# Kernel optimization log

Hardware: AMD Instinct MI355X
Metric: run time of the kernel (lower is better)

Reference implementation:

```python
import jax, jax.numpy as jnp
import numpy as np

B, T, IN, H, OUT = 256, 100, 128, 1024, 35
BITS = 4
SLOPE = 25.0
THR_H = 1.0
THR_O = 1.0
BETA1, BETA2, BETA3, BETA4 = 0.9, 0.85, 0.8, 0.95


def fake_quant(w, w_min, w_max, bits=BITS):
    # FakeQuantize in training mode: STE -> forward value is quantized, grad passes through clamp
    levels = 2 ** bits
    scale = (w_max - w_min) / (levels - 1)
    wc = jnp.clip(w, w_min, w_max)
    q = jnp.round((wc - w_min) / scale) * scale + w_min
    return wc + jax.lax.stop_gradient(q - wc)


@jax.custom_vjp
def spike(x):
    # Heaviside forward, fast-sigmoid surrogate backward (snn.surrogate.fast_sigmoid)
    return (x > 0).astype(x.dtype)

def _spike_fwd(x):
    return (x > 0).astype(x.dtype), x

def _spike_bwd(x, g):
    return (g / (SLOPE * jnp.abs(x) + 1.0) ** 2,)

spike.defvjp(_spike_fwd, _spike_bwd)


def lif_step(cur, mem, beta, thr, reset_mechanism):
    # snntorch Leaky (reset_delay semantics): reset computed from previous mem, detached
    reset = jax.lax.stop_gradient((mem > thr).astype(cur.dtype))
    base = beta * mem + cur
    if reset_mechanism == "subtract":
        mem_new = base - reset * thr
    else:  # "zero"
        mem_new = base - reset * base
    spk = spike(mem_new - thr)
    return spk, mem_new


def setup_inputs() -> dict:
    key = jax.random.key(0)
    ks = jax.random.split(key, 5)
    x = jax.random.normal(ks[0], (B, T, IN), dtype=jnp.float32)
    # QuantLinear init: uniform(w_min, w_max); fc1 uses (-0.5, 0.5), others (0.001, 1.0)
    w1 = jax.random.uniform(ks[1], (H, IN), minval=-0.5, maxval=0.5, dtype=jnp.float32)
    w2 = jax.random.uniform(ks[2], (H, H), minval=0.001, maxval=1.0, dtype=jnp.float32)
    w3 = jax.random.uniform(ks[3], (H, H), minval=0.001, maxval=1.0, dtype=jnp.float32)
    w4 = jax.random.uniform(ks[4], (OUT, H), minval=0.001, maxval=1.0, dtype=jnp.float32)
    return {"x": x, "w1": w1, "w2": w2, "w3": w3, "w4": w4}


def reference(x, w1, w2, w3, w4):
    # hoist weight quantization out of the time loop (identical math each step)
    q1 = fake_quant(w1, -0.5, 0.5)
    q2 = fake_quant(w2, 0.001, 1.0)
    q3 = fake_quant(w3, 0.001, 1.0)
    q4 = fake_quant(w4, 0.001, 1.0)
    xs = jnp.transpose(x, (1, 0, 2)) / 15.0  # [T, B, IN]
    Bx = x.shape[0]

    def step(carry, xt):
        m1, m2, m3, m4 = carry
        s1, m1 = lif_step(xt @ q1.T, m1, BETA1, THR_H, "subtract")
        s2, m2 = lif_step(s1 @ q2.T, m2, BETA2, THR_H, "subtract")
        s3, m3 = lif_step(s2 @ q3.T, m3, BETA3, THR_H, "subtract")
        s4, m4 = lif_step(s3 @ q4.T, m4, BETA4, THR_O, "zero")
        return (m1, m2, m3, m4), (s1, s2, s3, s4, m4)

    init = (jnp.zeros((Bx, H), x.dtype), jnp.zeros((Bx, H), x.dtype),
            jnp.zeros((Bx, H), x.dtype), jnp.zeros((Bx, OUT), x.dtype))
    _, (spk1, spk2, spk3, spk4, mem4) = jax.lax.scan(step, init, xs)
    # stacked along time dim 0, matching torch.stack(dim=0)
    return spk1, spk2, spk3, spk4, mem4
```

## Files before the change

kernel.cpp:

```cpp
#include <hip/hip_runtime.h>
#include <stdint.h>

#define NB  256
#define NT  100
#define NIN 128
#define NH  1024
#define NOUT 35

#define O_SPK2 26214400ull
#define O_SPK3 52428800ull
#define O_SPK4 78643200ull
#define O_MEM4 79539200ull

#define WS_XT   0ull
#define WS_Q1T  13107200ull
#define WS_K2T  13631488ull
#define WS_K3T  14680064ull
#define WS_K4T  15728640ull
#define WS_RS2  15777792ull
#define WS_RS3  15781888ull
#define WS_RS4  15785984ull

#define S2C ((float)((1.0 - 0.001) / 15.0))
#define S1C ((float)(1.0 / 15.0))

__global__ void k_prep(const float* __restrict__ x, const float* __restrict__ w1,
                       const float* __restrict__ w2, const float* __restrict__ w3,
                       const float* __restrict__ w4, uint8_t* __restrict__ ws)
{
  long long id = (long long)blockIdx.x * 256 + threadIdx.x;
  if (id < 1048576) {
    int i = (int)(id >> 10), j = (int)(id & 1023);
    float wv = w2[(size_t)j * 1024 + i];
    float wc = fminf(fmaxf(wv, 0.001f), 1.0f);
    ws[WS_K2T + id] = (uint8_t)(int)rintf((wc - 0.001f) / S2C);
    return;
  }
  id -= 1048576;
  if (id < 1048576) {
    int i = (int)(id >> 10), j = (int)(id & 1023);
    float wv = w3[(size_t)j * 1024 + i];
    float wc = fminf(fmaxf(wv, 0.001f), 1.0f);
    ws[WS_K3T + id] = (uint8_t)(int)rintf((wc - 0.001f) / S2C);
    return;
  }
  id -= 1048576;
  if (id < 49152) {
    int i = (int)(id / 48), j = (int)(id % 48);
    uint8_t v = 0;
    if (j < NOUT) {
      float wv = w4[(size_t)j * 1024 + i];
      float wc = fminf(fmaxf(wv, 0.001f), 1.0f);
      v = (uint8_t)(int)rintf((wc - 0.001f) / S2C);
    }
    ws[WS_K4T + id] = v;
    return;
  }
  id -= 49152;
  if (id < 131072) {
    int i = (int)(id >> 10), j = (int)(id & 1023);
    float wv = w1[(size_t)j * 128 + i];
    float wc = fminf(fmaxf(wv, -0.5f), 0.5f);
    float q = rintf((wc + 0.5f) / S1C) * S1C - 0.5f;
    ((float*)(ws + WS_Q1T))[id] = q;
    return;
  }
  id -= 131072;
  if (id < 3276800) {
    int row = (int)(id >> 7), i = (int)(id & 127);
    int tt = row >> 8, bb = row & 255;
    ((float*)(ws + WS_XT))[id] = x[((size_t)bb * NT + tt) * NIN + i] / 15.0f;
  }
}

__global__ void k_rowsum(const float* __restrict__ w2, const float* __restrict__ w3,
                         const float* __restrict__ w4, uint8_t* __restrict__ ws)
{
  int bid = blockIdx.x, tid = threadIdx.x;
  const float* W;
  uint32_t* o;
  if (bid < 1024)      { W = w2 + (size_t)bid * 1024;          o = (uint32_t*)(ws + WS_RS2) + bid; }
  else if (bid < 2048) { W = w3 + (size_t)(bid - 1024) * 1024; o = (uint32_t*)(ws + WS_RS3) + (bid - 1024); }
  else                 { W = w4 + (size_t)(bid - 2048) * 1024; o = (uint32_t*)(ws + WS_RS4) + (bid - 2048); }
  uint32_t s = 0;
  for (int i = tid; i < 1024; i += 256) {
    float wc = fminf(fmaxf(W[i], 0.001f), 1.0f);
    s += (uint32_t)(int)rintf((wc - 0.001f) / S2C);
  }
  #pragma unroll
  for (int off = 32; off; off >>= 1) s += (uint32_t)__shfl_down((int)s, off);
  __shared__ uint32_t red[4];
  if ((tid & 63) == 0) red[tid >> 6] = s;
  __syncthreads();
  if (tid == 0) *o = red[0] + red[1] + red[2] + red[3];
}

__global__ __launch_bounds__(512, 1) void k_spk1(const float* __restrict__ xt,
                                                 const float* __restrict__ q1T,
                                                 float* __restrict__ out)
{
  __shared__ float xs[25 * 128];
  const int b = blockIdx.x;
  const int tid = threadIdx.x;
  float m1a = 0.f, m1b = 0.f;

  for (int c = 0; c < 4; ++c) {
    __syncthreads();
    {
      int e = tid;
      int tt = e >> 5, iq = e & 31;
      ((float4*)xs)[e] = *(const float4*)(xt + ((size_t)(c * 25 + tt) * NB + b) * NIN + iq * 4);
      e = tid + 512;
      if (e < 800) {
        tt = e >> 5; iq = e & 31;
        ((float4*)xs)[e] = *(const float4*)(xt + ((size_t)(c * 25 + tt) * NB + b) * NIN + iq * 4);
      }
    }
    __syncthreads();

    float acc0[25], acc1[25];
    #pragma unroll
    for (int tt = 0; tt < 25; ++tt) { acc0[tt] = 0.f; acc1[tt] = 0.f; }

    for (int ib = 0; ib < 16; ++ib) {
      float q0[8], q1v[8];
      #pragma unroll
      for (int u = 0; u < 8; ++u) {
        q0[u]  = q1T[(size_t)(ib * 8 + u) * NH + tid];
        q1v[u] = q1T[(size_t)(ib * 8 + u) * NH + tid + 512];
      }
      #pragma unroll
      for (int tt = 0; tt < 25; ++tt) {
        const float4 xa = *(const float4*)&xs[tt * 128 + ib * 8];
        const float4 xb = *(const float4*)&xs[tt * 128 + ib * 8 + 4];
        acc0[tt] = fmaf(xa.x, q0[0], acc0[tt]);
        acc0[tt] = fmaf(xa.y, q0[1], acc0[tt]);
        acc0[tt] = fmaf(xa.z, q0[2], acc0[tt]);
        acc0[tt] = fmaf(xa.w, q0[3], acc0[tt]);
        acc0[tt] = fmaf(xb.x, q0[4], acc0[tt]);
        acc0[tt] = fmaf(xb.y, q0[5], acc0[tt]);
        acc0[tt] = fmaf(xb.z, q0[6], acc0[tt]);
        acc0[tt] = fmaf(xb.w, q0[7], acc0[tt]);
        acc1[tt] = fmaf(xa.x, q1v[0], acc1[tt]);
        acc1[tt] = fmaf(xa.y, q1v[1], acc1[tt]);
        acc1[tt] = fmaf(xa.z, q1v[2], acc1[tt]);
        acc1[tt] = fmaf(xa.w, q1v[3], acc1[tt]);
        acc1[tt] = fmaf(xb.x, q1v[4], acc1[tt]);
        acc1[tt] = fmaf(xb.y, q1v[5], acc1[tt]);
        acc1[tt] = fmaf(xb.z, q1v[6], acc1[tt]);
        acc1[tt] = fmaf(xb.w, q1v[7], acc1[tt]);
      }
    }
    #pragma unroll
    for (int tt = 0; tt < 25; ++tt) {
      const int t = c * 25 + tt;
      const size_t row = ((size_t)t * NB + b) * (size_t)NH;
      float rst0 = m1a > 1.0f ? 1.0f : 0.0f;
      m1a = fmaf(0.9f, m1a, acc0[tt]) - rst0;
      out[row + tid] = ((m1a - 1.0f) > 0.0f) ? 1.0f : 0.0f;
      float rst1 = m1b > 1.0f ? 1.0f : 0.0f;
      m1b = fmaf(0.9f, m1b, acc1[tt]) - rst1;
      out[row + tid + 512] = ((m1b - 1.0f) > 0.0f) ? 1.0f : 0.0f;
    }
  }
}

__global__ __launch_bounds__(1024, 1) void k_main(
    const uint8_t* __restrict__ k2T, const uint8_t* __restrict__ k3T,
    const uint8_t* __restrict__ k4T, const uint32_t* __restrict__ rs2,
    const uint32_t* __restrict__ rs3, const uint32_t* __restrict__ rs4,
    float* __restrict__ out)
{
  const int b = blockIdx.x;
  const int tid = threadIdx.x;
  const int lane = tid & 63;
  const int wave = tid >> 6;

  __shared__ uint16_t list[1024];
  __shared__ uint4    pEa4[1024];
  __shared__ uint4    pOa4[1024];
  __shared__ uint4    wcnt4[4];
  __shared__ uint32_t lpos;
  uint32_t* pEa  = (uint32_t*)pEa4;
  uint32_t* pOa  = (uint32_t*)pOa4;
  uint32_t* wcnt = (uint32_t*)wcnt4;

  float m2 = 0.f, m3 = 0.f, m4 = 0.f;
  const uint32_t r2v = rs2[tid];
  const uint32_t r3v = rs3[tid];
  const uint32_t r4v = (tid < NOUT) ? rs4[tid] : 0u;

  auto sumcnt = [&]() -> uint32_t {
    uint4 a0 = wcnt4[0], a1 = wcnt4[1], a2 = wcnt4[2], a3 = wcnt4[3];
    return a0.x + a0.y + a0.z + a0.w + a1.x + a1.y + a1.z + a1.w +
           a2.x + a2.y + a2.z + a2.w + a3.x + a3.y + a3.z + a3.w;
  };

  auto writeList = [&](uint64_t cw) {
    uint32_t cnt = (uint32_t)__popcll(cw);
    uint32_t bs = 0;
    if (lane == 0) bs = atomicAdd(&lpos, cnt);
    bs = (uint32_t)__shfl((int)bs, 0);
    if ((cw >> lane) & 1ull)
      list[bs + (uint32_t)__popcll(cw & ((1ull << lane) - 1ull))] = (uint16_t)tid;
  };

  auto gatherBig = [&](const uint8_t* __restrict__ mat, uint32_t nLv) {
    uint32_t aE0=0,aE1=0,aE2=0,aE3=0,aO0=0,aO1=0,aO2=0,aO3=0;
    const uint8_t* bp = mat + (lane << 4);
    uint32_t a = (uint32_t)wave;
    for (; a + 16 < nLv; a += 32) {
      uint32_t i0 = (uint32_t)__builtin_amdgcn_readfirstlane((int)list[a]);
      uint32_t i1 = (uint32_t)__builtin_amdgcn_readfirstlane((int)list[a + 16]);
      const uint4 w0 = *(const uint4*)(bp + ((size_t)i0 << 10));
      const uint4 w1 = *(const uint4*)(bp + ((size_t)i1 << 10));
      aE0 += w0.x & 0x00FF00FFu; aO0 += (w0.x >> 8) & 0x00FF00FFu;
      aE1 += w0.y & 0x00FF00FFu; aO1 += (w0.y >> 8) & 0x00FF00FFu;
      aE2 += w0.z & 0x00FF00FFu; aO2 += (w0.z >> 8) & 0x00FF00FFu;
      aE3 += w0.w & 0x00FF00FFu; aO3 += (w0.w >> 8) & 0x00FF00FFu;
      aE0 += w1.x & 0x00FF00FFu; aO0 += (w1.x >> 8) & 0x00FF00FFu;
      aE1 += w1.y & 0x00FF00FFu; aO1 += (w1.y >> 8) & 0x00FF00FFu;
      aE2 += w1.z & 0x00FF00FFu; aO2 += (w1.z >> 8) & 0x00FF00FFu;
      aE3 += w1.w & 0x00FF00FFu; aO3 += (w1.w >> 8) & 0x00FF00FFu;
    }
    if (a < nLv) {
      uint32_t i0 = (uint32_t)__builtin_amdgcn_readfirstlane((int)list[a]);
      const uint4 w0 = *(const uint4*)(bp + ((size_t)i0 << 10));
      aE0 += w0.x & 0x00FF00FFu; aO0 += (w0.x >> 8) & 0x00FF00FFu;
      aE1 += w0.y & 0x00FF00FFu; aO1 += (w0.y >> 8) & 0x00FF00FFu;
      aE2 += w0.z & 0x00FF00FFu; aO2 += (w0.z >> 8) & 0x00FF00FFu;
      aE3 += w0.w & 0x00FF00FFu; aO3 += (w0.w >> 8) & 0x00FF00FFu;
    }
    const int basei = (wave << 8) + (lane << 2);
    *(uint4*)&pEa[basei] = make_uint4(aE0, aE1, aE2, aE3);
    *(uint4*)&pOa[basei] = make_uint4(aO0, aO1, aO2, aO3);
  };

  auto gsum = [&](int jn) -> uint32_t {
    int w = jn >> 2, sh = (jn & 2) << 3;
    const uint32_t* P = (jn & 1) ? pOa : pEa;
    uint32_t s = 0;
    #pragma unroll
    for (int g = 0; g < 16; ++g) s += (P[(g << 8) + w] >> sh) & 0xffffu;
    return s;
  };

  float s1v = out[(size_t)b * NH + tid];
  uint32_t nT, nL; bool cm;

  for (int t = 0; t < NT; ++t) {
    const size_t rowH = ((size_t)t * NB + b) * (size_t)NH;
    const size_t rowO = ((size_t)t * NB + b) * (size_t)NOUT;

    bool sA = s1v > 0.5f;
    {
      int tn = (t + 1 < NT) ? (t + 1) : t;
      s1v = out[((size_t)tn * NB + b) * (size_t)NH + tid];
    }
    uint64_t b1 = __ballot(sA);
    if (tid == 0) lpos = 0;
    if (lane == 0) wcnt[wave] = (uint32_t)__popcll(b1);
    __syncthreads();
    nT = sumcnt(); cm = nT > 512; nL = cm ? 1024u - nT : nT;
    writeList(cm ? ~b1 : b1);
    __syncthreads();
    const uint32_t n1 = nT, nl1 = nL; const bool cm1 = cm;
    if (nl1) gatherBig(k2T, nl1);
    __syncthreads();

    bool sp;
    {
      uint32_t gsv = nl1 ? gsum(tid) : 0u;
      uint32_t K = cm1 ? (r2v - gsv) : gsv;
      float cur = fmaf(S2C, (float)K, 0.001f * (float)n1);
      float rst = m2 > 1.0f ? 1.0f : 0.0f;
      m2 = fmaf(0.85f, m2, cur) - rst;
      sp = (m2 - 1.0f) > 0.0f;
      out[O_SPK2 + rowH + tid] = sp ? 1.0f : 0.0f;
    }
    uint64_t b2 = __ballot(sp);
    if (tid == 0) lpos = 0;
    if (lane == 0) wcnt[wave] = (uint32_t)__popcll(b2);
    __syncthreads();
    nT = sumcnt(); cm = nT > 512; nL = cm ? 1024u - nT : nT;
    writeList(cm ? ~b2 : b2);
    __syncthreads();
    const uint32_t n2 = nT, nl2 = nL; const bool cm2 = cm;
    if (nl2) gatherBig(k3T, nl2);
    __syncthreads();

    {
      uint32_t gsv = nl2 ? gsum(tid) : 0u;
      uint32_t K = cm2 ? (r3v - gsv) : gsv;
      float cur = fmaf(S2C, (float)K, 0.001f * (float)n2);
      float rst = m3 > 1.0f ? 1.0f : 0.0f;
      m3 = fmaf(0.8f, m3, cur) - rst;
      sp = (m3 - 1.0f) > 0.0f;
      out[O_SPK3 + rowH + tid] = sp ? 1.0f : 0.0f;
    }
    uint64_t b3 = __ballot(sp);
    if (tid == 0) lpos = 0;
    if (lane == 0) wcnt[wave] = (uint32_t)__popcll(b3);
    __syncthreads();
    nT = sumcnt(); cm = nT > 512; nL = cm ? 1024u - nT : nT;
    writeList(cm ? ~b3 : b3);
    __syncthreads();
    const uint32_t n3 = nT, nl3 = nL; const bool cm3 = cm;

    if (nl3 && lane < 3) {
      uint32_t aE0=0,aE1=0,aE2=0,aE3=0,aO0=0,aO1=0,aO2=0,aO3=0;
      const uint8_t* bp = k4T + (lane << 4);
      for (uint32_t a = (uint32_t)wave; a < nl3; a += 16) {
        uint32_t i0 = (uint32_t)__builtin_amdgcn_readfirstlane((int)list[a]);
        const uint4 w0 = *(const uint4*)(bp + (size_t)i0 * 48u);
        aE0 += w0.x & 0x00FF00FFu; aO0 += (w0.x >> 8) & 0x00FF00FFu;
        aE1 += w0.y & 0x00FF00FFu; aO1 += (w0.y >> 8) & 0x00FF00FFu;
        aE2 += w0.z & 0x00FF00FFu; aO2 += (w0.z >> 8) & 0x00FF00FFu;
        aE3 += w0.w & 0x00FF00FFu; aO3 += (w0.w >> 8) & 0x00FF00FFu;
      }
      const int basei = (wave << 8) + (lane << 2);
      *(uint4*)&pEa[basei] = make_uint4(aE0, aE1, aE2, aE3);
      *(uint4*)&pOa[basei] = make_uint4(aO0, aO1, aO2, aO3);
    }
    __syncthreads();

    if (tid < NOUT) {
      uint32_t gsv = nl3 ? gsum(tid) : 0u;
      uint32_t K = cm3 ? (r4v - gsv) : gsv;
      float cur = fmaf(S2C, (float)K, 0.001f * (float)n3);
      float rst = m4 > 1.0f ? 1.0f : 0.0f;
      float bsv = fmaf(0.95f, m4, cur);
      m4 = (rst > 0.0f) ? 0.0f : bsv;
      out[O_SPK4 + rowO + tid] = ((m4 - 1.0f) > 0.0f) ? 1.0f : 0.0f;
      out[O_MEM4 + rowO + tid] = m4;
    }
  }
}

extern "C" void kernel_launch(void* const* d_in, const int* in_sizes, int n_in,
                              void* d_out, int out_size, void* d_ws, size_t ws_size,
                              hipStream_t stream)
{
  const float* x  = (const float*)d_in[0];
  const float* w1 = (const float*)d_in[1];
  const float* w2 = (const float*)d_in[2];
  const float* w3 = (const float*)d_in[3];
  const float* w4 = (const float*)d_in[4];
  float* out = (float*)d_out;
  uint8_t* ws = (uint8_t*)d_ws;
  hipLaunchKernelGGL(k_prep,   dim3(21696), dim3(256), 0, stream, x, w1, w2, w3, w4, ws);
  hipLaunchKernelGGL(k_rowsum, dim3(2083),  dim3(256), 0, stream, w2, w3, w4, ws);
  hipLaunchKernelGGL(k_spk1,   dim3(256),   dim3(512), 0, stream,
                     (const float*)(ws + WS_XT), (const float*)(ws + WS_Q1T), out);
  hipLaunchKernelGGL(k_main,   dim3(256),   dim3(1024), 0, stream,
                     ws + WS_K2T, ws + WS_K3T, ws + WS_K4T,
                     (const uint32_t*)(ws + WS_RS2), (const uint32_t*)(ws + WS_RS3),
                     (const uint32_t*)(ws + WS_RS4), out);
}
```

Before: 701.1 us.

## Halve main kernel block size, compute row sums in-kernel, replace atomic list build

The recurrent kernel now runs 512 threads per block, each owning two hidden neurons, so every gather step covers four list entries per wave with a stride of 8. The separate row-sum kernel is removed, and each block recomputes the quantized column sums at startup by gathering all rows of the weight tables. The shared-memory atomic list append is replaced by a deterministic prefix sum over the per-wave counts. This cuts one launch and the atomics and improves memory-level parallelism. In exchange it doubles per-thread work, halves the number of waves available to hide latency, and adds a redundant full-matrix sweep per block.

```diff
diff --git a/kernel.cpp b/kernel.cpp
--- a/kernel.cpp
+++ b/kernel.cpp
@@ -17,9 +17,6 @@
 #define WS_K2T  13631488ull
 #define WS_K3T  14680064ull
 #define WS_K4T  15728640ull
-#define WS_RS2  15777792ull
-#define WS_RS3  15781888ull
-#define WS_RS4  15785984ull
 
 #define S2C ((float)((1.0 - 0.001) / 15.0))
 #define S1C ((float)(1.0 / 15.0))
@@ -71,28 +68,6 @@
     int tt = row >> 8, bb = row & 255;
     ((float*)(ws + WS_XT))[id] = x[((size_t)bb * NT + tt) * NIN + i] / 15.0f;
   }
-}
-
-__global__ void k_rowsum(const float* __restrict__ w2, const float* __restrict__ w3,
-                         const float* __restrict__ w4, uint8_t* __restrict__ ws)
-{
-  int bid = blockIdx.x, tid = threadIdx.x;
-  const float* W;
-  uint32_t* o;
-  if (bid < 1024)      { W = w2 + (size_t)bid * 1024;          o = (uint32_t*)(ws + WS_RS2) + bid; }
-  else if (bid < 2048) { W = w3 + (size_t)(bid - 1024) * 1024; o = (uint32_t*)(ws + WS_RS3) + (bid - 1024); }
-  else                 { W = w4 + (size_t)(bid - 2048) * 1024; o = (uint32_t*)(ws + WS_RS4) + (bid - 2048); }
-  uint32_t s = 0;
-  for (int i = tid; i < 1024; i += 256) {
-    float wc = fminf(fmaxf(W[i], 0.001f), 1.0f);
-    s += (uint32_t)(int)rintf((wc - 0.001f) / S2C);
-  }
-  #pragma unroll
-  for (int off = 32; off; off >>= 1) s += (uint32_t)__shfl_down((int)s, off);
-  __shared__ uint32_t red[4];
-  if ((tid & 63) == 0) red[tid >> 6] = s;
-  __syncthreads();
-  if (tid == 0) *o = red[0] + red[1] + red[2] + red[3];
 }
 
 __global__ __launch_bounds__(512, 1) void k_spk1(const float* __restrict__ xt,
@@ -165,11 +140,15 @@
   }
 }
 
-__global__ __launch_bounds__(1024, 1) void k_main(
+#define ACC(V) do { \
+  aE0 += (V).x & 0x00FF00FFu; aO0 += ((V).x >> 8) & 0x00FF00FFu; \
+  aE1 += (V).y & 0x00FF00FFu; aO1 += ((V).y >> 8) & 0x00FF00FFu; \
+  aE2 += (V).z & 0x00FF00FFu; aO2 += ((V).z >> 8) & 0x00FF00FFu; \
+  aE3 += (V).w & 0x00FF00FFu; aO3 += ((V).w >> 8) & 0x00FF00FFu; } while (0)
+
+__global__ __launch_bounds__(512, 1) void k_main(
     const uint8_t* __restrict__ k2T, const uint8_t* __restrict__ k3T,
-    const uint8_t* __restrict__ k4T, const uint32_t* __restrict__ rs2,
-    const uint32_t* __restrict__ rs3, const uint32_t* __restrict__ rs4,
-    float* __restrict__ out)
+    const uint8_t* __restrict__ k4T, float* __restrict__ out)
 {
   const int b = blockIdx.x;
   const int tid = threadIdx.x;
@@ -177,151 +156,207 @@
   const int wave = tid >> 6;
 
   __shared__ uint16_t list[1024];
-  __shared__ uint4    pEa4[1024];
-  __shared__ uint4    pOa4[1024];
-  __shared__ uint4    wcnt4[4];
-  __shared__ uint32_t lpos;
+  __shared__ uint4    pEa4[512];
+  __shared__ uint4    pOa4[512];
+  __shared__ uint4    wcnt4[2];
   uint32_t* pEa  = (uint32_t*)pEa4;
   uint32_t* pOa  = (uint32_t*)pOa4;
   uint32_t* wcnt = (uint32_t*)wcnt4;
 
-  float m2 = 0.f, m3 = 0.f, m4 = 0.f;
-  const uint32_t r2v = rs2[tid];
-  const uint32_t r3v = rs3[tid];
-  const uint32_t r4v = (tid < NOUT) ? rs4[tid] : 0u;
-
-  auto sumcnt = [&]() -> uint32_t {
-    uint4 a0 = wcnt4[0], a1 = wcnt4[1], a2 = wcnt4[2], a3 = wcnt4[3];
-    return a0.x + a0.y + a0.z + a0.w + a1.x + a1.y + a1.z + a1.w +
-           a2.x + a2.y + a2.z + a2.w + a3.x + a3.y + a3.z + a3.w;
-  };
-
-  auto writeList = [&](uint64_t cw) {
-    uint32_t cnt = (uint32_t)__popcll(cw);
-    uint32_t bs = 0;
-    if (lane == 0) bs = atomicAdd(&lpos, cnt);
-    bs = (uint32_t)__shfl((int)bs, 0);
-    if ((cw >> lane) & 1ull)
-      list[bs + (uint32_t)__popcll(cw & ((1ull << lane) - 1ull))] = (uint16_t)tid;
+  float m2[2] = {0.f, 0.f}, m3[2] = {0.f, 0.f}, m4 = 0.f;
+  uint32_t nT, nL; bool cm;
+
+  auto buildList = [&](uint64_t bA, uint64_t bB) {
+    const uint4 c0 = wcnt4[0], c1 = wcnt4[1];
+    nT = c0.x + c0.y + c0.z + c0.w + c1.x + c1.y + c1.z + c1.w;
+    cm = nT > 512;
+    nL = cm ? (1024u - nT) : nT;
+    uint32_t pre = 0;
+    pre += (wave > 0) ? c0.x : 0u;  pre += (wave > 1) ? c0.y : 0u;
+    pre += (wave > 2) ? c0.z : 0u;  pre += (wave > 3) ? c0.w : 0u;
+    pre += (wave > 4) ? c1.x : 0u;  pre += (wave > 5) ? c1.y : 0u;
+    pre += (wave > 6) ? c1.z : 0u;
+    const uint32_t bs = cm ? ((uint32_t)(wave << 7) - pre) : pre;
+    const uint64_t cA = cm ? ~bA : bA;
+    const uint64_t cB = cm ? ~bB : bB;
+    const uint64_t ltm = (1ull << lane) - 1ull;
+    if ((cA >> lane) & 1ull)
+      list[bs + (uint32_t)__popcll(cA & ltm)] = (uint16_t)tid;
+    if ((cB >> lane) & 1ull)
+      list[bs + (uint32_t)__popcll(cA) + (uint32_t)__popcll(cB & ltm)] = (uint16_t)(tid + 512);
   };
 
   auto gatherBig = [&](const uint8_t* __restrict__ mat, uint32_t nLv) {
     uint32_t aE0=0,aE1=0,aE2=0,aE3=0,aO0=0,aO1=0,aO2=0,aO3=0;
     const uint8_t* bp = mat + (lane << 4);
     uint32_t a = (uint32_t)wave;
-    for (; a + 16 < nLv; a += 32) {
+    for (; a + 24 < nLv; a += 32) {
       uint32_t i0 = (uint32_t)__builtin_amdgcn_readfirstlane((int)list[a]);
-      uint32_t i1 = (uint32_t)__builtin_amdgcn_readfirstlane((int)list[a + 16]);
-      const uint4 w0 = *(const uint4*)(bp + ((size_t)i0 << 10));
-      const uint4 w1 = *(const uint4*)(bp + ((size_t)i1 << 10));
-      aE0 += w0.x & 0x00FF00FFu; aO0 += (w0.x >> 8) & 0x00FF00FFu;
-      aE1 += w0.y & 0x00FF00FFu; aO1 += (w0.y >> 8) & 0x00FF00FFu;
-      aE2 += w0.z & 0x00FF00FFu; aO2 += (w0.z >> 8) & 0x00FF00FFu;
-      aE3 += w0.w & 0x00FF00FFu; aO3 += (w0.w >> 8) & 0x00FF00FFu;
-      aE0 += w1.x & 0x00FF00FFu; aO0 += (w1.x >> 8) & 0x00FF00FFu;
-      aE1 += w1.y & 0x00FF00FFu; aO1 += (w1.y >> 8) & 0x00FF00FFu;
-      aE2 += w1.z & 0x00FF00FFu; aO2 += (w1.z >> 8) & 0x00FF00FFu;
-      aE3 += w1.w & 0x00FF00FFu; aO3 += (w1.w >> 8) & 0x00FF00FFu;
-    }
-    if (a < nLv) {
+      uint32_t i1 = (uint32_t)__builtin_amdgcn_readfirstlane((int)list[a + 8]);
+      uint32_t i2 = (uint32_t)__builtin_amdgcn_readfirstlane((int)list[a + 16]);
+      uint32_t i3 = (uint32_t)__builtin_amdgcn_readfirstlane((int)list[a + 24]);
+      const uint4 v0 = *(const uint4*)(bp + ((size_t)i0 << 10));
+      const uint4 v1 = *(const uint4*)(bp + ((size_t)i1 << 10));
+      const uint4 v2 = *(const uint4*)(bp + ((size_t)i2 << 10));
+      const uint4 v3 = *(const uint4*)(bp + ((size_t)i3 << 10));
+      ACC(v0); ACC(v1); ACC(v2); ACC(v3);
+    }
+    for (; a < nLv; a += 8) {
       uint32_t i0 = (uint32_t)__builtin_amdgcn_readfirstlane((int)list[a]);
-      const uint4 w0 = *(const uint4*)(bp + ((size_t)i0 << 10));
-      aE0 += w0.x & 0x00FF00FFu; aO0 += (w0.x >> 8) & 0x00FF00FFu;
-      aE1 += w0.y & 0x00FF00FFu; aO1 += (w0.y >> 8) & 0x00FF00FFu;
-      aE2 += w0.z & 0x00FF00FFu; aO2 += (w0.z >> 8) & 0x00FF00FFu;
-      aE3 += w0.w & 0x00FF00FFu; aO3 += (w0.w >> 8) & 0x00FF00FFu;
+      const uint4 v0 = *(const uint4*)(bp + ((size_t)i0 << 10));
+      ACC(v0);
     }
     const int basei = (wave << 8) + (lane << 2);
     *(uint4*)&pEa[basei] = make_uint4(aE0, aE1, aE2, aE3);
     *(uint4*)&pOa[basei] = make_uint4(aO0, aO1, aO2, aO3);
   };
 
+  auto gatherAll = [&](const uint8_t* __restrict__ mat) {
+    uint32_t aE0=0,aE1=0,aE2=0,aE3=0,aO0=0,aO1=0,aO2=0,aO3=0;
+    const uint8_t* bp = mat + (lane << 4);
+    for (uint32_t a = (uint32_t)wave; a + 24 < 1024u; a += 32) {
+      const uint4 v0 = *(const uint4*)(bp + ((size_t)a << 10));
+      const uint4 v1 = *(const uint4*)(bp + ((size_t)(a + 8) << 10));
+      const uint4 v2 = *(const uint4*)(bp + ((size_t)(a + 16) << 10));
+      const uint4 v3 = *(const uint4*)(bp + ((size_t)(a + 24) << 10));
+      ACC(v0); ACC(v1); ACC(v2); ACC(v3);
+    }
+    const int basei = (wave << 8) + (lane << 2);
+    *(uint4*)&pEa[basei] = make_uint4(aE0, aE1, aE2, aE3);
+    *(uint4*)&pOa[basei] = make_uint4(aO0, aO1, aO2, aO3);
+  };
+
+  auto gather4 = [&](uint32_t nLv) {
+    uint32_t aE0=0,aE1=0,aE2=0,aE3=0,aO0=0,aO1=0,aO2=0,aO3=0;
+    const uint8_t* bp = k4T + (lane << 4);
+    uint32_t a = (uint32_t)wave;
+    for (; a + 24 < nLv; a += 32) {
+      uint32_t i0 = (uint32_t)__builtin_amdgcn_readfirstlane((int)list[a]);
+      uint32_t i1 = (uint32_t)__builtin_amdgcn_readfirstlane((int)list[a + 8]);
+      uint32_t i2 = (uint32_t)__builtin_amdgcn_readfirstlane((int)list[a + 16]);
+      uint32_t i3 = (uint32_t)__builtin_amdgcn_readfirstlane((int)list[a + 24]);
+      const uint4 v0 = *(const uint4*)(bp + (size_t)i0 * 48u);
+      const uint4 v1 = *(const uint4*)(bp + (size_t)i1 * 48u);
+      const uint4 v2 = *(const uint4*)(bp + (size_t)i2 * 48u);
+      const uint4 v3 = *(const uint4*)(bp + (size_t)i3 * 48u);
+      ACC(v0); ACC(v1); ACC(v2); ACC(v3);
+    }
+    for (; a < nLv; a += 8) {
+      uint32_t i0 = (uint32_t)__builtin_amdgcn_readfirstlane((int)list[a]);
+      const uint4 v0 = *(const uint4*)(bp + (size_t)i0 * 48u);
+      ACC(v0);
+    }
+    const int basei = (wave << 8) + (lane << 2);
+    *(uint4*)&pEa[basei] = make_uint4(aE0, aE1, aE2, aE3);
+    *(uint4*)&pOa[basei] = make_uint4(aO0, aO1, aO2, aO3);
+  };
+
+  auto gather4All = [&]() {
+    uint32_t aE0=0,aE1=0,aE2=0,aE3=0,aO0=0,aO1=0,aO2=0,aO3=0;
+    const uint8_t* bp = k4T + (lane << 4);
+    for (uint32_t a = (uint32_t)wave; a + 24 < 1024u; a += 32) {
+      const uint4 v0 = *(const uint4*)(bp + (size_t)a * 48u);
+      const uint4 v1 = *(const uint4*)(bp + (size_t)(a + 8) * 48u);
+      const uint4 v2 = *(const uint4*)(bp + (size_t)(a + 16) * 48u);
+      const uint4 v3 = *(const uint4*)(bp + (size_t)(a + 24) * 48u);
+      ACC(v0); ACC(v1); ACC(v2); ACC(v3);
+    }
+    const int basei = (wave << 8) + (lane << 2);
+    *(uint4*)&pEa[basei] = make_uint4(aE0, aE1, aE2, aE3);
+    *(uint4*)&pOa[basei] = make_uint4(aO0, aO1, aO2, aO3);
+  };
+
   auto gsum = [&](int jn) -> uint32_t {
-    int w = jn >> 2, sh = (jn & 2) << 3;
+    const int w = jn >> 2, sh = (jn & 2) << 3;
     const uint32_t* P = (jn & 1) ? pOa : pEa;
     uint32_t s = 0;
     #pragma unroll
-    for (int g = 0; g < 16; ++g) s += (P[(g << 8) + w] >> sh) & 0xffffu;
-    return s;
-  };
-
-  float s1v = out[(size_t)b * NH + tid];
-  uint32_t nT, nL; bool cm;
+    for (int g = 0; g < 8; ++g) s += P[(g << 8) + w];
+    return (s >> sh) & 0xffffu;
+  };
+
+  gatherAll(k2T);
+  __syncthreads();
+  uint32_t r2[2]; r2[0] = gsum(tid); r2[1] = gsum(tid + 512);
+  __syncthreads();
+  gatherAll(k3T);
+  __syncthreads();
+  uint32_t r3[2]; r3[0] = gsum(tid); r3[1] = gsum(tid + 512);
+  __syncthreads();
+  if (lane < 3) gather4All();
+  __syncthreads();
+  const uint32_t r4v = (tid < NOUT) ? gsum(tid) : 0u;
+
+  float s1a = out[(size_t)b * NH + tid];
+  float s1b = out[(size_t)b * NH + tid + 512];
 
   for (int t = 0; t < NT; ++t) {
     const size_t rowH = ((size_t)t * NB + b) * (size_t)NH;
     const size_t rowO = ((size_t)t * NB + b) * (size_t)NOUT;
 
-    bool sA = s1v > 0.5f;
+    bool sA = s1a > 0.5f, sB = s1b > 0.5f;
     {
       int tn = (t + 1 < NT) ? (t + 1) : t;
-      s1v = out[((size_t)tn * NB + b) * (size_t)NH + tid];
-    }
-    uint64_t b1 = __ballot(sA);
-    if (tid == 0) lpos = 0;
-    if (lane == 0) wcnt[wave] = (uint32_t)__popcll(b1);
-    __syncthreads();
-    nT = sumcnt(); cm = nT > 512; nL = cm ? 1024u - nT : nT;
-    writeList(cm ? ~b1 : b1);
+      size_t rowN = ((size_t)tn * NB + b) * (size_t)NH;
+      s1a = out[rowN + tid];
+      s1b = out[rowN + tid + 512];
+    }
+    uint64_t bA = __ballot(sA), bB = __ballot(sB);
+    if (lane == 0) wcnt[wave] = (uint32_t)(__popcll(bA) + __popcll(bB));
+    __syncthreads();
+    buildList(bA, bB);
     __syncthreads();
     const uint32_t n1 = nT, nl1 = nL; const bool cm1 = cm;
     if (nl1) gatherBig(k2T, nl1);
     __syncthreads();
 
-    bool sp;
     {
-      uint32_t gsv = nl1 ? gsum(tid) : 0u;
-      uint32_t K = cm1 ? (r2v - gsv) : gsv;
-      float cur = fmaf(S2C, (float)K, 0.001f * (float)n1);
-      float rst = m2 > 1.0f ? 1.0f : 0.0f;
-      m2 = fmaf(0.85f, m2, cur) - rst;
-      sp = (m2 - 1.0f) > 0.0f;
-      out[O_SPK2 + rowH + tid] = sp ? 1.0f : 0.0f;
-    }
-    uint64_t b2 = __ballot(sp);
-    if (tid == 0) lpos = 0;
-    if (lane == 0) wcnt[wave] = (uint32_t)__popcll(b2);
-    __syncthreads();
-    nT = sumcnt(); cm = nT > 512; nL = cm ? 1024u - nT : nT;
-    writeList(cm ? ~b2 : b2);
+      float nb = 0.001f * (float)n1;
+      #pragma unroll
+      for (int c = 0; c < 2; ++c) {
+        int j = (c << 9) + tid;
+        uint32_t gsv = nl1 ? gsum(j) : 0u;
+        uint32_t K = cm1 ? (r2[c] - gsv) : gsv;
+        float cur = fmaf(S2C, (float)K, nb);
+        float rst = m2[c] > 1.0f ? 1.0f : 0.0f;
+        m2[c] = fmaf(0.85f, m2[c], cur) - rst;
+        bool sp = (m2[c] - 1.0f) > 0.0f;
+        out[O_SPK2 + rowH + j] = sp ? 1.0f : 0.0f;
+        if (c == 0) sA = sp; else sB = sp;
+      }
+    }
+    bA = __ballot(sA); bB = __ballot(sB);
+    if (lane == 0) wcnt[wave] = (uint32_t)(__popcll(bA) + __popcll(bB));
+    __syncthreads();
+    buildList(bA, bB);
     __syncthreads();
     const uint32_t n2 = nT, nl2 = nL; const bool cm2 = cm;
     if (nl2) gatherBig(k3T, nl2);
     __syncthreads();
 
     {
-      uint32_t gsv = nl2 ? gsum(tid) : 0u;
-      uint32_t K = cm2 ? (r3v - gsv) : gsv;
-      float cur = fmaf(S2C, (float)K, 0.001f * (float)n2);
-      float rst = m3 > 1.0f ? 1.0f : 0.0f;
-      m3 = fmaf(0.8f, m3, cur) - rst;
-      sp = (m3 - 1.0f) > 0.0f;
-      out[O_SPK3 + rowH + tid] = sp ? 1.0f : 0.0f;
-    }
-    uint64_t b3 = __ballot(sp);
-    if (tid == 0) lpos = 0;
-    if (lane == 0) wcnt[wave] = (uint32_t)__popcll(b3);
-    __syncthreads();
-    nT = sumcnt(); cm = nT > 512; nL = cm ? 1024u - nT : nT;
-    writeList(cm ? ~b3 : b3);
+      float nb = 0.001f * (float)n2;
+      #pragma unroll
+      for (int c = 0; c < 2; ++c) {
+        int j = (c << 9) + tid;
+        uint32_t gsv = nl2 ? gsum(j) : 0u;
+        uint32_t K = cm2 ? (r3[c] - gsv) : gsv;
+        float cur = fmaf(S2C, (float)K, nb);
+        float rst = m3[c] > 1.0f ? 1.0f : 0.0f;
+        m3[c] = fmaf(0.8f, m3[c], cur) - rst;
+        bool sp = (m3[c] - 1.0f) > 0.0f;
+        out[O_SPK3 + rowH + j] = sp ? 1.0f : 0.0f;
+        if (c == 0) sA = sp; else sB = sp;
+      }
+    }
+    bA = __ballot(sA); bB = __ballot(sB);
+    if (lane == 0) wcnt[wave] = (uint32_t)(__popcll(bA) + __popcll(bB));
+    __syncthreads();
+    buildList(bA, bB);
     __syncthreads();
     const uint32_t n3 = nT, nl3 = nL; const bool cm3 = cm;
 
-    if (nl3 && lane < 3) {
-      uint32_t aE0=0,aE1=0,aE2=0,aE3=0,aO0=0,aO1=0,aO2=0,aO3=0;
-      const uint8_t* bp = k4T + (lane << 4);
-      for (uint32_t a = (uint32_t)wave; a < nl3; a += 16) {
-        uint32_t i0 = (uint32_t)__builtin_amdgcn_readfirstlane((int)list[a]);
-        const uint4 w0 = *(const uint4*)(bp + (size_t)i0 * 48u);
-        aE0 += w0.x & 0x00FF00FFu; aO0 += (w0.x >> 8) & 0x00FF00FFu;
-        aE1 += w0.y & 0x00FF00FFu; aO1 += (w0.y >> 8) & 0x00FF00FFu;
-        aE2 += w0.z & 0x00FF00FFu; aO2 += (w0.z >> 8) & 0x00FF00FFu;
-        aE3 += w0.w & 0x00FF00FFu; aO3 += (w0.w >> 8) & 0x00FF00FFu;
-      }
-      const int basei = (wave << 8) + (lane << 2);
-      *(uint4*)&pEa[basei] = make_uint4(aE0, aE1, aE2, aE3);
-      *(uint4*)&pOa[basei] = make_uint4(aO0, aO1, aO2, aO3);
-    }
+    if (nl3 && lane < 3) gather4(nl3);
     __syncthreads();
 
     if (tid < NOUT) {
@@ -336,6 +371,7 @@
     }
   }
 }
+#undef ACC
 
 extern "C" void kernel_launch(void* const* d_in, const int* in_sizes, int n_in,
                               void* d_out, int out_size, void* d_ws, size_t ws_size,
@@ -348,12 +384,9 @@
   const float* w4 = (const float*)d_in[4];
   float* out = (float*)d_out;
   uint8_t* ws = (uint8_t*)d_ws;
-  hipLaunchKernelGGL(k_prep,   dim3(21696), dim3(256), 0, stream, x, w1, w2, w3, w4, ws);
-  hipLaunchKernelGGL(k_rowsum, dim3(2083),  dim3(256), 0, stream, w2, w3, w4, ws);
-  hipLaunchKernelGGL(k_spk1,   dim3(256),   dim3(512), 0, stream,
+  hipLaunchKernelGGL(k_prep, dim3(21696), dim3(256), 0, stream, x, w1, w2, w3, w4, ws);
+  hipLaunchKernelGGL(k_spk1, dim3(256),   dim3(512), 0, stream,
                      (const float*)(ws + WS_XT), (const float*)(ws + WS_Q1T), out);
-  hipLaunchKernelGGL(k_main,   dim3(256),   dim3(1024), 0, stream,
-                     ws + WS_K2T, ws + WS_K3T, ws + WS_K4T,
-                     (const uint32_t*)(ws + WS_RS2), (const uint32_t*)(ws + WS_RS3),
-                     (const uint32_t*)(ws + WS_RS4), out);
+  hipLaunchKernelGGL(k_main, dim3(256),   dim3(512), 0, stream,
+                     ws + WS_K2T, ws + WS_K3T, ws + WS_K4T, out);
 }
```

After: 693.2 us. No clear change (-1.1%).
